# Kernel tuning notes

Hardware: AMD Instinct MI355X
Metric: run time of the kernel (lower is better)

The kernel has to match this reference:

```python
import jax, jax.numpy as jnp
import numpy as np

N_NODES = 100000
N_EDGES = 1600000
N_FEAT = 128
HIDDEN = 64
N_LAYERS = 3


def setup_inputs() -> dict:
    key = jax.random.key(0)
    ks = jax.random.split(key, 8)
    x = jax.random.normal(ks[0], (N_NODES, N_FEAT), dtype=jnp.float32)
    edge_index = jax.random.randint(ks[1], (2, N_EDGES), 0, N_NODES, dtype=jnp.int64)
    s_emb = 1.0 / np.sqrt(N_FEAT)
    s_h = 1.0 / np.sqrt(HIDDEN)
    W_emb = jax.random.uniform(ks[2], (N_FEAT, HIDDEN), jnp.float32, -s_emb, s_emb)
    b_emb = jax.random.uniform(ks[3], (HIDDEN,), jnp.float32, -s_emb, s_emb)
    Ws = jax.random.uniform(ks[4], (N_LAYERS, HIDDEN, HIDDEN), jnp.float32, -s_h, s_h)
    bs = jax.random.uniform(ks[5], (N_LAYERS, HIDDEN), jnp.float32, -s_h, s_h)
    return {"x": x, "edge_index": edge_index, "W_emb": W_emb, "b_emb": b_emb,
            "Ws": Ws, "bs": bs}


def gcn_conv(h, src, dst, W, b, deg_inv_sqrt):
    # GCNConv with self-loops and symmetric normalization (PyG semantics):
    # out_i = sum_{j->i} d_i^{-1/2} d_j^{-1/2} (h_j W) + d_i^{-1} (h_i W) + b
    hw = h @ W                                   # [N, H]
    norm = deg_inv_sqrt[src] * deg_inv_sqrt[dst]  # [E]
    msg = hw[src] * norm[:, None]                 # [E, H] gather
    agg = jax.ops.segment_sum(msg, dst, num_segments=N_NODES)  # scatter-add
    agg = agg + hw * (deg_inv_sqrt * deg_inv_sqrt)[:, None]    # self-loop term
    return agg + b


def reference(x, edge_index, W_emb, b_emb, Ws, bs):
    src, dst = edge_index[0], edge_index[1]
    # degree with self-loops (edge weight 1), shared by every layer
    deg = jnp.zeros((N_NODES,), x.dtype).at[dst].add(1.0) + 1.0
    deg_inv_sqrt = jax.lax.rsqrt(deg)

    h = x @ W_emb + b_emb  # embedding Linear
    for i in range(N_LAYERS):
        h = jax.nn.relu(gcn_conv(h, src, dst, Ws[i], bs[i], deg_inv_sqrt))
    return h
```

## Files before the change

### kernel.cpp

```cpp
#include <hip/hip_runtime.h>
#include <hip/hip_fp16.h>
#include <math.h>

#define NN 100000
#define NE 1600000
#define NF 128
#define NH 64
#define NBUCK 196
#define CHA 8192
#define CAP 10240

__global__ __launch_bounds__(256) void zero_bcnt(int* bcnt) {
    int t = threadIdx.x;
    if (t < NBUCK) bcnt[t] = 0;
}

__global__ __launch_bounds__(256) void part_bucket2(const int* __restrict__ src,
                                                    const int* __restrict__ dst,
                                                    int* __restrict__ bcnt,
                                                    int* __restrict__ tmp, int E) {
    __shared__ int hist[NBUCK];
    __shared__ int base[NBUCK];
    int t = threadIdx.x;
    int e0 = blockIdx.x * CHA;
    int e1 = min(e0 + CHA, E);
    if (t < NBUCK) hist[t] = 0;
    __syncthreads();
    for (int i = e0 + t; i < e1; i += 256) {
        atomicAdd(&hist[dst[i] >> 9], 1);
    }
    __syncthreads();
    if (t < NBUCK) {
        int h = hist[t];
        base[t] = h ? atomicAdd(&bcnt[t], h) : 0;
        hist[t] = 0;
    }
    __syncthreads();
    for (int i = e0 + t; i < e1; i += 256) {
        int d = dst[i];
        int b = d >> 9;
        int r = atomicAdd(&hist[b], 1);
        tmp[b * CAP + base[b] + r] = ((d & 511) << 17) | src[i];
    }
}

__global__ __launch_bounds__(256) void scan_buckets(const int* __restrict__ bcnt,
                                                    int* __restrict__ cbase,
                                                    int* __restrict__ rowptr) {
    __shared__ int s[256];
    int t = threadIdx.x;
    s[t] = (t < NBUCK) ? bcnt[t] : 0;
    __syncthreads();
    for (int off = 1; off < 256; off <<= 1) {
        int v = (t >= off) ? s[t - off] : 0;
        __syncthreads();
        s[t] += v;
        __syncthreads();
    }
    if (t < NBUCK) cbase[t] = (t == 0) ? 0 : s[t - 1];
    if (t == 0) rowptr[NN] = NE;
}

__global__ __launch_bounds__(256) void bucket_finalize(const int* __restrict__ bcnt,
                                                       const int* __restrict__ cbase,
                                                       const int* __restrict__ tmp,
                                                       int* __restrict__ rowptr,
                                                       float* __restrict__ dsq,
                                                       int* __restrict__ csr_src) {
    __shared__ int ebuf[CAP];
    __shared__ int hcnt[512];
    __shared__ int hoff[512];
    __shared__ int s[256];
    int b = blockIdx.x, t = threadIdx.x;
    int cb = bcnt[b];
    int base = cbase[b];
    const int* tsrc = tmp + b * CAP;
    for (int i = t; i < cb; i += 256) ebuf[i] = tsrc[i];
    hcnt[t] = 0;
    hcnt[t + 256] = 0;
    __syncthreads();
    for (int i = t; i < cb; i += 256) atomicAdd(&hcnt[ebuf[i] >> 17], 1);
    __syncthreads();
    int c0 = hcnt[2 * t], c1 = hcnt[2 * t + 1];
    s[t] = c0 + c1;
    __syncthreads();
    for (int off = 1; off < 256; off <<= 1) {
        int v = (t >= off) ? s[t - off] : 0;
        __syncthreads();
        s[t] += v;
        __syncthreads();
    }
    int pb = (t == 0) ? 0 : s[t - 1];
    hoff[2 * t] = pb;
    hoff[2 * t + 1] = pb + c0;
    __syncthreads();
    int nodelo = b << 9;
    int nnodes = min(512, NN - nodelo);
    for (int i = t; i < nnodes; i += 256) {
        rowptr[nodelo + i] = base + hoff[i];
        dsq[nodelo + i] = rsqrtf((float)hcnt[i] + 1.0f);
    }
    __syncthreads();
    for (int i = t; i < cb; i += 256) {
        int e = ebuf[i];
        int dlow = e >> 17;
        int p = atomicAdd(&hoff[dlow], 1);
        csr_src[base + p] = e & 0x1FFFF;
    }
}

__global__ __launch_bounds__(256) void combine_w(const float* __restrict__ We,
                                                 const float* __restrict__ be,
                                                 const float* __restrict__ W0,
                                                 float* __restrict__ Wc,
                                                 float* __restrict__ bc) {
    __shared__ float w0[NH * NH];
    int t = threadIdx.x;
    for (int i = t; i < NH * NH; i += 256) w0[i] = W0[i];
    __syncthreads();
    int row = blockIdx.x * 4 + (t >> 6);
    int col = t & 63;
    float a = 0.f;
#pragma unroll 8
    for (int k = 0; k < NH; ++k) a += We[row * NH + k] * w0[k * NH + col];
    Wc[row * NH + col] = a;
    if (blockIdx.x == 0 && t < NH) {
        float s = 0.f;
        for (int k = 0; k < NH; ++k) s += be[k] * w0[k * NH + t];
        bc[t] = s;
    }
}

__global__ __launch_bounds__(256) void fuse0_gemm(const float* __restrict__ x,
                                                  const float* __restrict__ Wc,
                                                  const float* __restrict__ bc,
                                                  const float* __restrict__ dsq,
                                                  __half* __restrict__ hws) {
    __shared__ float tile[16 * NF];
    __shared__ float red[4][16][NH];
    int t = threadIdx.x;
    int lane = t & 63;
    int wave = __builtin_amdgcn_readfirstlane(t >> 6);
    int row0 = blockIdx.x * 16;

    const float4* xsrc = (const float4*)(x + (size_t)row0 * NF);
    float4* t4 = (float4*)tile;
    t4[t] = xsrc[t];
    t4[t + 256] = xsrc[t + 256];

    float Wreg[32];
#pragma unroll
    for (int kk = 0; kk < 32; ++kk) Wreg[kk] = Wc[(wave * 32 + kk) * NH + lane];
    __syncthreads();

    float acc[16];
#pragma unroll
    for (int r = 0; r < 16; ++r) {
        const float4* rp = (const float4*)(tile + r * NF + wave * 32);
        float a = 0.f;
#pragma unroll
        for (int q = 0; q < 8; ++q) {
            float4 v = rp[q];
            a += v.x * Wreg[q * 4 + 0];
            a += v.y * Wreg[q * 4 + 1];
            a += v.z * Wreg[q * 4 + 2];
            a += v.w * Wreg[q * 4 + 3];
        }
        acc[r] = a;
    }
#pragma unroll
    for (int r = 0; r < 16; ++r) red[wave][r][lane] = acc[r];
    __syncthreads();
#pragma unroll
    for (int i = 0; i < 4; ++i) {
        int o = i * 256 + t;
        int r = o >> 6, c = o & 63;
        float s = red[0][r][c] + red[1][r][c] + red[2][r][c] + red[3][r][c];
        int row = row0 + r;
        hws[(size_t)row * NH + c] = __float2half((s + bc[c]) * dsq[row]);
    }
}

__global__ __launch_bounds__(256) void layer_gemm(const float* __restrict__ h,
                                                  const float* __restrict__ W,
                                                  const float* __restrict__ dsq,
                                                  __half* __restrict__ hws) {
    __shared__ float tile[16 * NH];
    __shared__ float red[4][16][NH];
    int t = threadIdx.x;
    int lane = t & 63;
    int wave = __builtin_amdgcn_readfirstlane(t >> 6);
    int row0 = blockIdx.x * 16;

    const float4* hsrc = (const float4*)(h + (size_t)row0 * NH);
    float4* t4 = (float4*)tile;
    t4[t] = hsrc[t];

    float Wreg[16];
#pragma unroll
    for (int kk = 0; kk < 16; ++kk) Wreg[kk] = W[(wave * 16 + kk) * NH + lane];
    __syncthreads();

    float acc[16];
#pragma unroll
    for (int r = 0; r < 16; ++r) {
        const float4* rp = (const float4*)(tile + r * NH + wave * 16);
        float a = 0.f;
#pragma unroll
        for (int q = 0; q < 4; ++q) {
            float4 v = rp[q];
            a += v.x * Wreg[q * 4 + 0];
            a += v.y * Wreg[q * 4 + 1];
            a += v.z * Wreg[q * 4 + 2];
            a += v.w * Wreg[q * 4 + 3];
        }
        acc[r] = a;
    }
#pragma unroll
    for (int r = 0; r < 16; ++r) red[wave][r][lane] = acc[r];
    __syncthreads();
#pragma unroll
    for (int i = 0; i < 4; ++i) {
        int o = i * 256 + t;
        int r = o >> 6, c = o & 63;
        float s = red[0][r][c] + red[1][r][c] + red[2][r][c] + red[3][r][c];
        int row = row0 + r;
        hws[(size_t)row * NH + c] = __float2half(s * dsq[row]);
    }
}

__global__ __launch_bounds__(256) void gather_agg(const int* __restrict__ rowptr,
                                                  const int* __restrict__ csr_src,
                                                  const __half* __restrict__ hws,
                                                  const float* __restrict__ dsq,
                                                  const float* __restrict__ b,
                                                  float* __restrict__ outbuf, int n) {
    int node = blockIdx.x * 4 + (threadIdx.x >> 6);
    int lane = threadIdx.x & 63;
    if (node >= n) return;
    int g  = lane >> 3;
    int fl = (lane & 7) << 3;
    int beg = rowptr[node], end = rowptr[node + 1];

    float a0 = 0.f, a1 = 0.f, a2 = 0.f, a3 = 0.f;
    float a4 = 0.f, a5 = 0.f, a6 = 0.f, a7 = 0.f;

#define ADDROW(sidx)                                                         \
    {                                                                        \
        uint4 rv = *(const uint4*)(hws + (size_t)(sidx) * NH + fl);          \
        float2 f0 = __half22float2(*(const __half2*)&rv.x);                  \
        float2 f1 = __half22float2(*(const __half2*)&rv.y);                  \
        float2 f2 = __half22float2(*(const __half2*)&rv.z);                  \
        float2 f3 = __half22float2(*(const __half2*)&rv.w);                  \
        a0 += f0.x; a1 += f0.y; a2 += f1.x; a3 += f1.y;                      \
        a4 += f2.x; a5 += f2.y; a6 += f3.x; a7 += f3.y;                      \
    }

    if (g == 0) ADDROW(node);
    int jend = beg + ((end - beg) & ~7);
#pragma unroll 2
    for (int j = beg; j < jend; j += 8) {
        int s = csr_src[j + g];
        ADDROW(s);
    }
    if (jend + g < end) {
        int s = csr_src[jend + g];
        ADDROW(s);
    }
#undef ADDROW

    a0 += __shfl_xor(a0, 8);  a1 += __shfl_xor(a1, 8);
    a2 += __shfl_xor(a2, 8);  a3 += __shfl_xor(a3, 8);
    a4 += __shfl_xor(a4, 8);  a5 += __shfl_xor(a5, 8);
    a6 += __shfl_xor(a6, 8);  a7 += __shfl_xor(a7, 8);
    a0 += __shfl_xor(a0, 16); a1 += __shfl_xor(a1, 16);
    a2 += __shfl_xor(a2, 16); a3 += __shfl_xor(a3, 16);
    a4 += __shfl_xor(a4, 16); a5 += __shfl_xor(a5, 16);
    a6 += __shfl_xor(a6, 16); a7 += __shfl_xor(a7, 16);
    a0 += __shfl_xor(a0, 32); a1 += __shfl_xor(a1, 32);
    a2 += __shfl_xor(a2, 32); a3 += __shfl_xor(a3, 32);
    a4 += __shfl_xor(a4, 32); a5 += __shfl_xor(a5, 32);
    a6 += __shfl_xor(a6, 32); a7 += __shfl_xor(a7, 32);

    if (lane < 8) {
        float ds = dsq[node];
        float4 b0 = *(const float4*)(b + fl);
        float4 b1 = *(const float4*)(b + fl + 4);
        float4 o0, o1;
        o0.x = fmaxf(ds * a0 + b0.x, 0.f);
        o0.y = fmaxf(ds * a1 + b0.y, 0.f);
        o0.z = fmaxf(ds * a2 + b0.z, 0.f);
        o0.w = fmaxf(ds * a3 + b0.w, 0.f);
        o1.x = fmaxf(ds * a4 + b1.x, 0.f);
        o1.y = fmaxf(ds * a5 + b1.y, 0.f);
        o1.z = fmaxf(ds * a6 + b1.z, 0.f);
        o1.w = fmaxf(ds * a7 + b1.w, 0.f);
        *(float4*)(outbuf + (size_t)node * NH + fl) = o0;
        *(float4*)(outbuf + (size_t)node * NH + fl + 4) = o1;
    }
}

extern "C" void kernel_launch(void* const* d_in, const int* in_sizes, int n_in,
                              void* d_out, int out_size, void* d_ws, size_t ws_size,
                              hipStream_t stream) {
    const float* x     = (const float*)d_in[0];
    const int*   ei    = (const int*)d_in[1];
    const float* W_emb = (const float*)d_in[2];
    const float* b_emb = (const float*)d_in[3];
    const float* Ws    = (const float*)d_in[4];
    const float* bs    = (const float*)d_in[5];
    float* out = (float*)d_out;

    const int* src = ei;
    const int* dst = ei + NE;

    char* w = (char*)d_ws;
    int*    bcnt     = (int*)w;               w += 256 * 4;
    int*    cbase    = (int*)w;               w += 256 * 4;
    int*    rowptr   = (int*)w;               w += (NN + 1) * 4;
    float*  dsq      = (float*)w;             w += NN * 4;
    float*  Wc       = (float*)w;             w += NF * NH * 4;
    float*  bc       = (float*)w;             w += NH * 4;
    int*    csr_src  = (int*)w;               w += NE * 4;
    int*    tmp      = (int*)w;               w += (size_t)NBUCK * CAP * 4;
    float*  A        = (float*)w;             w += (size_t)NN * NH * 4;
    __half* Bh       = (__half*)w;

    zero_bcnt<<<1, 256, 0, stream>>>(bcnt);
    part_bucket2<<<(NE + CHA - 1) / CHA, 256, 0, stream>>>(src, dst, bcnt, tmp, NE);
    scan_buckets<<<1, 256, 0, stream>>>(bcnt, cbase, rowptr);
    bucket_finalize<<<NBUCK, 256, 0, stream>>>(bcnt, cbase, tmp, rowptr, dsq, csr_src);

    combine_w<<<NF / 4, 256, 0, stream>>>(W_emb, b_emb, Ws, Wc, bc);

    fuse0_gemm<<<NN / 16, 256, 0, stream>>>(x, Wc, bc, dsq, Bh);
    gather_agg<<<(NN + 3) / 4, 256, 0, stream>>>(rowptr, csr_src, Bh,
                                                 dsq, bs, A, NN);

    for (int l = 1; l < 3; ++l) {
        layer_gemm<<<NN / 16, 256, 0, stream>>>(A, Ws + l * NH * NH, dsq, Bh);
        float* dbuf = (l == 2) ? out : A;
        gather_agg<<<(NN + 3) / 4, 256, 0, stream>>>(rowptr, csr_src, Bh,
                                                     dsq, bs + l * NH, dbuf, NN);
    }
}
```

Before: 295.8 us.

## Fuse next-layer GEMM into gather epilogue and double fuse0 tile rows

The separate layer_gemm kernels are removed. Each gather block now loads the next layer's 64x64 weight into LDS, writes the relu'd aggregated rows to LDS, and computes the next layer's pre-scaled fp16 features directly. This removes the fp32 intermediate write and re-read and two kernel launches per layer. The cost is a 16KB weight load into LDS for every 4-node block and a block-wide sync, which may hurt occupancy. fuse0_gemm also processes 32 rows per block instead of 16.

```diff
diff --git a/kernel.cpp b/kernel.cpp
--- a/kernel.cpp
+++ b/kernel.cpp
@@ -136,26 +136,26 @@
                                                   const float* __restrict__ bc,
                                                   const float* __restrict__ dsq,
                                                   __half* __restrict__ hws) {
-    __shared__ float tile[16 * NF];
-    __shared__ float red[4][16][NH];
+    __shared__ float tile[32 * NF];
+    __shared__ float red[4][32][NH];
     int t = threadIdx.x;
     int lane = t & 63;
     int wave = __builtin_amdgcn_readfirstlane(t >> 6);
-    int row0 = blockIdx.x * 16;
+    int row0 = blockIdx.x * 32;
 
     const float4* xsrc = (const float4*)(x + (size_t)row0 * NF);
     float4* t4 = (float4*)tile;
-    t4[t] = xsrc[t];
-    t4[t + 256] = xsrc[t + 256];
+#pragma unroll
+    for (int i = 0; i < 4; ++i) t4[t + i * 256] = xsrc[t + i * 256];
 
     float Wreg[32];
 #pragma unroll
     for (int kk = 0; kk < 32; ++kk) Wreg[kk] = Wc[(wave * 32 + kk) * NH + lane];
     __syncthreads();
 
-    float acc[16];
-#pragma unroll
-    for (int r = 0; r < 16; ++r) {
+    float acc[32];
+#pragma unroll
+    for (int r = 0; r < 32; ++r) {
         const float4* rp = (const float4*)(tile + r * NF + wave * 32);
         float a = 0.f;
 #pragma unroll
@@ -169,10 +169,10 @@
         acc[r] = a;
     }
 #pragma unroll
-    for (int r = 0; r < 16; ++r) red[wave][r][lane] = acc[r];
-    __syncthreads();
-#pragma unroll
-    for (int i = 0; i < 4; ++i) {
+    for (int r = 0; r < 32; ++r) red[wave][r][lane] = acc[r];
+    __syncthreads();
+#pragma unroll
+    for (int i = 0; i < 8; ++i) {
         int o = i * 256 + t;
         int r = o >> 6, c = o & 63;
         float s = red[0][r][c] + red[1][r][c] + red[2][r][c] + red[3][r][c];
@@ -181,73 +181,41 @@
     }
 }
 
-__global__ __launch_bounds__(256) void layer_gemm(const float* __restrict__ h,
-                                                  const float* __restrict__ W,
-                                                  const float* __restrict__ dsq,
-                                                  __half* __restrict__ hws) {
-    __shared__ float tile[16 * NH];
-    __shared__ float red[4][16][NH];
-    int t = threadIdx.x;
-    int lane = t & 63;
-    int wave = __builtin_amdgcn_readfirstlane(t >> 6);
-    int row0 = blockIdx.x * 16;
-
-    const float4* hsrc = (const float4*)(h + (size_t)row0 * NH);
-    float4* t4 = (float4*)tile;
-    t4[t] = hsrc[t];
-
-    float Wreg[16];
-#pragma unroll
-    for (int kk = 0; kk < 16; ++kk) Wreg[kk] = W[(wave * 16 + kk) * NH + lane];
-    __syncthreads();
-
-    float acc[16];
-#pragma unroll
-    for (int r = 0; r < 16; ++r) {
-        const float4* rp = (const float4*)(tile + r * NH + wave * 16);
-        float a = 0.f;
-#pragma unroll
-        for (int q = 0; q < 4; ++q) {
-            float4 v = rp[q];
-            a += v.x * Wreg[q * 4 + 0];
-            a += v.y * Wreg[q * 4 + 1];
-            a += v.z * Wreg[q * 4 + 2];
-            a += v.w * Wreg[q * 4 + 3];
-        }
-        acc[r] = a;
-    }
-#pragma unroll
-    for (int r = 0; r < 16; ++r) red[wave][r][lane] = acc[r];
-    __syncthreads();
-#pragma unroll
-    for (int i = 0; i < 4; ++i) {
-        int o = i * 256 + t;
-        int r = o >> 6, c = o & 63;
-        float s = red[0][r][c] + red[1][r][c] + red[2][r][c] + red[3][r][c];
-        int row = row0 + r;
-        hws[(size_t)row * NH + c] = __float2half(s * dsq[row]);
-    }
-}
-
-__global__ __launch_bounds__(256) void gather_agg(const int* __restrict__ rowptr,
-                                                  const int* __restrict__ csr_src,
-                                                  const __half* __restrict__ hws,
-                                                  const float* __restrict__ dsq,
-                                                  const float* __restrict__ b,
-                                                  float* __restrict__ outbuf, int n) {
-    int node = blockIdx.x * 4 + (threadIdx.x >> 6);
-    int lane = threadIdx.x & 63;
-    if (node >= n) return;
-    int g  = lane >> 3;
-    int fl = (lane & 7) << 3;
-    int beg = rowptr[node], end = rowptr[node + 1];
-
-    float a0 = 0.f, a1 = 0.f, a2 = 0.f, a3 = 0.f;
-    float a4 = 0.f, a5 = 0.f, a6 = 0.f, a7 = 0.f;
+#define GATHER_BODY                                                          \
+    int t = threadIdx.x;                                                     \
+    int node = blockIdx.x * 4 + (t >> 6);                                    \
+    int lane = t & 63;                                                       \
+    int g = lane >> 3;                                                       \
+    int fl = (lane & 7) << 3;                                                \
+    int beg = rowptr[node], end = rowptr[node + 1];                          \
+    float a0 = 0.f, a1 = 0.f, a2 = 0.f, a3 = 0.f;                            \
+    float a4 = 0.f, a5 = 0.f, a6 = 0.f, a7 = 0.f;                            \
+    if (g == 0) ADDROW(node);                                                \
+    int jend = beg + ((end - beg) & ~7);                                     \
+    _Pragma("unroll 2") for (int j = beg; j < jend; j += 8) {                \
+        int s_ = csr_src[j + g];                                             \
+        ADDROW(s_);                                                          \
+    }                                                                        \
+    if (jend + g < end) {                                                    \
+        int s_ = csr_src[jend + g];                                          \
+        ADDROW(s_);                                                          \
+    }                                                                        \
+    a0 += __shfl_xor(a0, 8);  a1 += __shfl_xor(a1, 8);                       \
+    a2 += __shfl_xor(a2, 8);  a3 += __shfl_xor(a3, 8);                       \
+    a4 += __shfl_xor(a4, 8);  a5 += __shfl_xor(a5, 8);                       \
+    a6 += __shfl_xor(a6, 8);  a7 += __shfl_xor(a7, 8);                       \
+    a0 += __shfl_xor(a0, 16); a1 += __shfl_xor(a1, 16);                      \
+    a2 += __shfl_xor(a2, 16); a3 += __shfl_xor(a3, 16);                      \
+    a4 += __shfl_xor(a4, 16); a5 += __shfl_xor(a5, 16);                      \
+    a6 += __shfl_xor(a6, 16); a7 += __shfl_xor(a7, 16);                      \
+    a0 += __shfl_xor(a0, 32); a1 += __shfl_xor(a1, 32);                      \
+    a2 += __shfl_xor(a2, 32); a3 += __shfl_xor(a3, 32);                      \
+    a4 += __shfl_xor(a4, 32); a5 += __shfl_xor(a5, 32);                      \
+    a6 += __shfl_xor(a6, 32); a7 += __shfl_xor(a7, 32);
 
 #define ADDROW(sidx)                                                         \
     {                                                                        \
-        uint4 rv = *(const uint4*)(hws + (size_t)(sidx) * NH + fl);          \
+        uint4 rv = *(const uint4*)(hws_in + (size_t)(sidx) * NH + fl);       \
         float2 f0 = __half22float2(*(const __half2*)&rv.x);                  \
         float2 f1 = __half22float2(*(const __half2*)&rv.y);                  \
         float2 f2 = __half22float2(*(const __half2*)&rv.z);                  \
@@ -256,32 +224,58 @@
         a4 += f2.x; a5 += f2.y; a6 += f3.x; a7 += f3.y;                      \
     }
 
-    if (g == 0) ADDROW(node);
-    int jend = beg + ((end - beg) & ~7);
-#pragma unroll 2
-    for (int j = beg; j < jend; j += 8) {
-        int s = csr_src[j + g];
-        ADDROW(s);
-    }
-    if (jend + g < end) {
-        int s = csr_src[jend + g];
-        ADDROW(s);
-    }
-#undef ADDROW
-
-    a0 += __shfl_xor(a0, 8);  a1 += __shfl_xor(a1, 8);
-    a2 += __shfl_xor(a2, 8);  a3 += __shfl_xor(a3, 8);
-    a4 += __shfl_xor(a4, 8);  a5 += __shfl_xor(a5, 8);
-    a6 += __shfl_xor(a6, 8);  a7 += __shfl_xor(a7, 8);
-    a0 += __shfl_xor(a0, 16); a1 += __shfl_xor(a1, 16);
-    a2 += __shfl_xor(a2, 16); a3 += __shfl_xor(a3, 16);
-    a4 += __shfl_xor(a4, 16); a5 += __shfl_xor(a5, 16);
-    a6 += __shfl_xor(a6, 16); a7 += __shfl_xor(a7, 16);
-    a0 += __shfl_xor(a0, 32); a1 += __shfl_xor(a1, 32);
-    a2 += __shfl_xor(a2, 32); a3 += __shfl_xor(a3, 32);
-    a4 += __shfl_xor(a4, 32); a5 += __shfl_xor(a5, 32);
-    a6 += __shfl_xor(a6, 32); a7 += __shfl_xor(a7, 32);
-
+__global__ __launch_bounds__(256) void gather_gemm(const int* __restrict__ rowptr,
+                                                   const int* __restrict__ csr_src,
+                                                   const __half* __restrict__ hws_in,
+                                                   const float* __restrict__ dsq,
+                                                   const float* __restrict__ b,
+                                                   const float* __restrict__ Wn,
+                                                   __half* __restrict__ hws_out) {
+    __shared__ float w_lds[NH * NH];
+    __shared__ float h_lds[4][NH];
+    {
+        const float4* ws = (const float4*)Wn;
+        float4* wd = (float4*)w_lds;
+        int tt = threadIdx.x;
+#pragma unroll
+        for (int i = 0; i < 4; ++i) wd[tt + i * 256] = ws[tt + i * 256];
+    }
+    GATHER_BODY
+    float ds = dsq[node];
+    if (lane < 8) {
+        float4 b0 = *(const float4*)(b + fl);
+        float4 b1 = *(const float4*)(b + fl + 4);
+        float4 h0, h1;
+        h0.x = fmaxf(ds * a0 + b0.x, 0.f);
+        h0.y = fmaxf(ds * a1 + b0.y, 0.f);
+        h0.z = fmaxf(ds * a2 + b0.z, 0.f);
+        h0.w = fmaxf(ds * a3 + b0.w, 0.f);
+        h1.x = fmaxf(ds * a4 + b1.x, 0.f);
+        h1.y = fmaxf(ds * a5 + b1.y, 0.f);
+        h1.z = fmaxf(ds * a6 + b1.z, 0.f);
+        h1.w = fmaxf(ds * a7 + b1.w, 0.f);
+        *(float4*)&h_lds[t >> 6][fl] = h0;
+        *(float4*)&h_lds[t >> 6][fl + 4] = h1;
+    }
+    __syncthreads();
+    int r = t >> 6, c = lane;
+    float acc = 0.f;
+#pragma unroll
+    for (int k = 0; k < NH; k += 4) {
+        float4 hv = *(const float4*)&h_lds[r][k];
+        acc += hv.x * w_lds[k * NH + c] + hv.y * w_lds[(k + 1) * NH + c] +
+               hv.z * w_lds[(k + 2) * NH + c] + hv.w * w_lds[(k + 3) * NH + c];
+    }
+    hws_out[(size_t)node * NH + c] = __float2half(acc * ds);
+}
+
+__global__ __launch_bounds__(256) void gather_final(const int* __restrict__ rowptr,
+                                                    const int* __restrict__ csr_src,
+                                                    const __half* __restrict__ hws_in,
+                                                    const float* __restrict__ dsq,
+                                                    const float* __restrict__ b,
+                                                    float* __restrict__ outbuf) {
+    GATHER_BODY
     if (lane < 8) {
         float ds = dsq[node];
         float4 b0 = *(const float4*)(b + fl);
@@ -323,8 +317,8 @@
     float*  bc       = (float*)w;             w += NH * 4;
     int*    csr_src  = (int*)w;               w += NE * 4;
     int*    tmp      = (int*)w;               w += (size_t)NBUCK * CAP * 4;
-    float*  A        = (float*)w;             w += (size_t)NN * NH * 4;
-    __half* Bh       = (__half*)w;
+    __half* Bh0      = (__half*)w;            w += (size_t)NN * NH * 2;
+    __half* Bh1      = (__half*)w;
 
     zero_bcnt<<<1, 256, 0, stream>>>(bcnt);
     part_bucket2<<<(NE + CHA - 1) / CHA, 256, 0, stream>>>(src, dst, bcnt, tmp, NE);
@@ -333,14 +327,12 @@
 
     combine_w<<<NF / 4, 256, 0, stream>>>(W_emb, b_emb, Ws, Wc, bc);
 
-    fuse0_gemm<<<NN / 16, 256, 0, stream>>>(x, Wc, bc, dsq, Bh);
-    gather_agg<<<(NN + 3) / 4, 256, 0, stream>>>(rowptr, csr_src, Bh,
-                                                 dsq, bs, A, NN);
-
-    for (int l = 1; l < 3; ++l) {
-        layer_gemm<<<NN / 16, 256, 0, stream>>>(A, Ws + l * NH * NH, dsq, Bh);
-        float* dbuf = (l == 2) ? out : A;
-        gather_agg<<<(NN + 3) / 4, 256, 0, stream>>>(rowptr, csr_src, Bh,
-                                                     dsq, bs + l * NH, dbuf, NN);
-    }
-}
+    fuse0_gemm<<<NN / 32, 256, 0, stream>>>(x, Wc, bc, dsq, Bh0);
+
+    gather_gemm<<<NN / 4, 256, 0, stream>>>(rowptr, csr_src, Bh0, dsq, bs,
+                                            Ws + 1 * NH * NH, Bh1);
+    gather_gemm<<<NN / 4, 256, 0, stream>>>(rowptr, csr_src, Bh1, dsq, bs + NH,
+                                            Ws + 2 * NH * NH, Bh0);
+    gather_final<<<NN / 4, 256, 0, stream>>>(rowptr, csr_src, Bh0, dsq,
+                                             bs + 2 * NH, out);
+}
```

Result: slower. 311.0 us (+5.1%).

## Store intermediate activations in fp16 and batch neighbor index loads via shuffles

Applied to the files above, without the earlier changes.

Intermediate layer activations between gather and GEMM are now stored as fp16 instead of fp32, halving that write and read traffic. The gather kernel loads up to 64 neighbor indices per wave in one coalesced load and distributes them with shuffles, masking the tail instead of running a separate remainder path. The zero kernel is replaced by hipMemsetAsync. This adds an extra rounding to fp16 of the post-ReLU activations, which costs some accuracy.

```diff
diff --git a/kernel.cpp b/kernel.cpp
--- a/kernel.cpp
+++ b/kernel.cpp
@@ -9,11 +9,6 @@
 #define NBUCK 196
 #define CHA 8192
 #define CAP 10240
-
-__global__ __launch_bounds__(256) void zero_bcnt(int* bcnt) {
-    int t = threadIdx.x;
-    if (t < NBUCK) bcnt[t] = 0;
-}
 
 __global__ __launch_bounds__(256) void part_bucket2(const int* __restrict__ src,
                                                     const int* __restrict__ dst,
@@ -181,7 +176,7 @@
     }
 }
 
-__global__ __launch_bounds__(256) void layer_gemm(const float* __restrict__ h,
+__global__ __launch_bounds__(256) void layer_gemm(const __half* __restrict__ h,
                                                   const float* __restrict__ W,
                                                   const float* __restrict__ dsq,
                                                   __half* __restrict__ hws) {
@@ -192,9 +187,13 @@
     int wave = __builtin_amdgcn_readfirstlane(t >> 6);
     int row0 = blockIdx.x * 16;
 
-    const float4* hsrc = (const float4*)(h + (size_t)row0 * NH);
-    float4* t4 = (float4*)tile;
-    t4[t] = hsrc[t];
+    {
+        uint2 v = ((const uint2*)(h + (size_t)row0 * NH))[t];
+        float2 p0 = __half22float2(*(const __half2*)&v.x);
+        float2 p1 = __half22float2(*(const __half2*)&v.y);
+        float4 f = make_float4(p0.x, p0.y, p1.x, p1.y);
+        *(float4*)&tile[t * 4] = f;
+    }
 
     float Wreg[16];
 #pragma unroll
@@ -229,59 +228,91 @@
     }
 }
 
-__global__ __launch_bounds__(256) void gather_agg(const int* __restrict__ rowptr,
-                                                  const int* __restrict__ csr_src,
-                                                  const __half* __restrict__ hws,
-                                                  const float* __restrict__ dsq,
-                                                  const float* __restrict__ b,
-                                                  float* __restrict__ outbuf, int n) {
-    int node = blockIdx.x * 4 + (threadIdx.x >> 6);
-    int lane = threadIdx.x & 63;
-    if (node >= n) return;
-    int g  = lane >> 3;
-    int fl = (lane & 7) << 3;
-    int beg = rowptr[node], end = rowptr[node + 1];
-
-    float a0 = 0.f, a1 = 0.f, a2 = 0.f, a3 = 0.f;
-    float a4 = 0.f, a5 = 0.f, a6 = 0.f, a7 = 0.f;
-
-#define ADDROW(sidx)                                                         \
+#define ADDROWM(sidx, m)                                                     \
     {                                                                        \
-        uint4 rv = *(const uint4*)(hws + (size_t)(sidx) * NH + fl);          \
+        uint4 rv = *(const uint4*)(hws_in + (size_t)(sidx) * NH + fl);       \
         float2 f0 = __half22float2(*(const __half2*)&rv.x);                  \
         float2 f1 = __half22float2(*(const __half2*)&rv.y);                  \
         float2 f2 = __half22float2(*(const __half2*)&rv.z);                  \
         float2 f3 = __half22float2(*(const __half2*)&rv.w);                  \
-        a0 += f0.x; a1 += f0.y; a2 += f1.x; a3 += f1.y;                      \
-        a4 += f2.x; a5 += f2.y; a6 += f3.x; a7 += f3.y;                      \
-    }
-
-    if (g == 0) ADDROW(node);
-    int jend = beg + ((end - beg) & ~7);
-#pragma unroll 2
-    for (int j = beg; j < jend; j += 8) {
-        int s = csr_src[j + g];
-        ADDROW(s);
-    }
-    if (jend + g < end) {
-        int s = csr_src[jend + g];
-        ADDROW(s);
-    }
-#undef ADDROW
-
-    a0 += __shfl_xor(a0, 8);  a1 += __shfl_xor(a1, 8);
-    a2 += __shfl_xor(a2, 8);  a3 += __shfl_xor(a3, 8);
-    a4 += __shfl_xor(a4, 8);  a5 += __shfl_xor(a5, 8);
-    a6 += __shfl_xor(a6, 8);  a7 += __shfl_xor(a7, 8);
-    a0 += __shfl_xor(a0, 16); a1 += __shfl_xor(a1, 16);
-    a2 += __shfl_xor(a2, 16); a3 += __shfl_xor(a3, 16);
-    a4 += __shfl_xor(a4, 16); a5 += __shfl_xor(a5, 16);
-    a6 += __shfl_xor(a6, 16); a7 += __shfl_xor(a7, 16);
-    a0 += __shfl_xor(a0, 32); a1 += __shfl_xor(a1, 32);
-    a2 += __shfl_xor(a2, 32); a3 += __shfl_xor(a3, 32);
-    a4 += __shfl_xor(a4, 32); a5 += __shfl_xor(a5, 32);
+        a0 += f0.x * (m); a1 += f0.y * (m); a2 += f1.x * (m); a3 += f1.y * (m); \
+        a4 += f2.x * (m); a5 += f2.y * (m); a6 += f3.x * (m); a7 += f3.y * (m); \
+    }
+
+#define GATHER_BODY                                                          \
+    int t = threadIdx.x;                                                     \
+    int node = blockIdx.x * 4 + (t >> 6);                                    \
+    int lane = t & 63;                                                       \
+    int g = lane >> 3;                                                       \
+    int fl = (lane & 7) << 3;                                                \
+    int beg = rowptr[node], end = rowptr[node + 1];                          \
+    int deg = end - beg;                                                     \
+    float a0 = 0.f, a1 = 0.f, a2 = 0.f, a3 = 0.f;                            \
+    float a4 = 0.f, a5 = 0.f, a6 = 0.f, a7 = 0.f;                            \
+    if (g == 0) ADDROWM(node, 1.f);                                          \
+    int idxl = csr_src[min(beg + lane, NE - 1)];                             \
+    _Pragma("unroll")                                                        \
+    for (int k = 0; k < 8; ++k) {                                            \
+        if (k * 8 < deg) {                                                   \
+            int e = k * 8 + g;                                               \
+            int s_ = __shfl(idxl, min(e, deg - 1));                          \
+            float m = (e < deg) ? 1.f : 0.f;                                 \
+            ADDROWM(s_, m);                                                  \
+        }                                                                    \
+    }                                                                        \
+    for (int jb = beg + 64; jb < end; jb += 64) {       \
+        int rem = end - jb;                                                  \
+        int idx2 = csr_src[min(jb + lane, NE - 1)];                          \
+        _Pragma("unroll")                                                    \
+        for (int k = 0; k < 8; ++k) {                                        \
+            if (k * 8 < rem) {                                               \
+                int e = k * 8 + g;                                           \
+                int s_ = __shfl(idx2, min(e, rem - 1));                      \
+                float m = (e < rem) ? 1.f : 0.f;                             \
+                ADDROWM(s_, m);                                              \
+            }                                                                \
+        }                                                                    \
+    }                                                                        \
+    a0 += __shfl_xor(a0, 8);  a1 += __shfl_xor(a1, 8);                       \
+    a2 += __shfl_xor(a2, 8);  a3 += __shfl_xor(a3, 8);                       \
+    a4 += __shfl_xor(a4, 8);  a5 += __shfl_xor(a5, 8);                       \
+    a6 += __shfl_xor(a6, 8);  a7 += __shfl_xor(a7, 8);                       \
+    a0 += __shfl_xor(a0, 16); a1 += __shfl_xor(a1, 16);                      \
+    a2 += __shfl_xor(a2, 16); a3 += __shfl_xor(a3, 16);                      \
+    a4 += __shfl_xor(a4, 16); a5 += __shfl_xor(a5, 16);                      \
+    a6 += __shfl_xor(a6, 16); a7 += __shfl_xor(a7, 16);                      \
+    a0 += __shfl_xor(a0, 32); a1 += __shfl_xor(a1, 32);                      \
+    a2 += __shfl_xor(a2, 32); a3 += __shfl_xor(a3, 32);                      \
+    a4 += __shfl_xor(a4, 32); a5 += __shfl_xor(a5, 32);                      \
     a6 += __shfl_xor(a6, 32); a7 += __shfl_xor(a7, 32);
 
+__global__ __launch_bounds__(256) void gather_h(const int* __restrict__ rowptr,
+                                                const int* __restrict__ csr_src,
+                                                const __half* __restrict__ hws_in,
+                                                const float* __restrict__ dsq,
+                                                const float* __restrict__ b,
+                                                __half* __restrict__ hout) {
+    GATHER_BODY
+    if (lane < 8) {
+        float ds = dsq[node];
+        float4 b0 = *(const float4*)(b + fl);
+        float4 b1 = *(const float4*)(b + fl + 4);
+        __half2 o[4];
+        o[0] = __floats2half2_rn(fmaxf(ds * a0 + b0.x, 0.f), fmaxf(ds * a1 + b0.y, 0.f));
+        o[1] = __floats2half2_rn(fmaxf(ds * a2 + b0.z, 0.f), fmaxf(ds * a3 + b0.w, 0.f));
+        o[2] = __floats2half2_rn(fmaxf(ds * a4 + b1.x, 0.f), fmaxf(ds * a5 + b1.y, 0.f));
+        o[3] = __floats2half2_rn(fmaxf(ds * a6 + b1.z, 0.f), fmaxf(ds * a7 + b1.w, 0.f));
+        *(uint4*)(hout + (size_t)node * NH + fl) = *(const uint4*)o;
+    }
+}
+
+__global__ __launch_bounds__(256) void gather_out(const int* __restrict__ rowptr,
+                                                  const int* __restrict__ csr_src,
+                                                  const __half* __restrict__ hws_in,
+                                                  const float* __restrict__ dsq,
+                                                  const float* __restrict__ b,
+                                                  float* __restrict__ outbuf) {
+    GATHER_BODY
     if (lane < 8) {
         float ds = dsq[node];
         float4 b0 = *(const float4*)(b + fl);
@@ -323,10 +354,10 @@
     float*  bc       = (float*)w;             w += NH * 4;
     int*    csr_src  = (int*)w;               w += NE * 4;
     int*    tmp      = (int*)w;               w += (size_t)NBUCK * CAP * 4;
-    float*  A        = (float*)w;             w += (size_t)NN * NH * 4;
-    __half* Bh       = (__half*)w;
-
-    zero_bcnt<<<1, 256, 0, stream>>>(bcnt);
+    __half* Bh       = (__half*)w;            w += (size_t)NN * NH * 2;
+    __half* H16      = (__half*)w;
+
+    hipMemsetAsync(bcnt, 0, 256 * 4, stream);
     part_bucket2<<<(NE + CHA - 1) / CHA, 256, 0, stream>>>(src, dst, bcnt, tmp, NE);
     scan_buckets<<<1, 256, 0, stream>>>(bcnt, cbase, rowptr);
     bucket_finalize<<<NBUCK, 256, 0, stream>>>(bcnt, cbase, tmp, rowptr, dsq, csr_src);
@@ -334,13 +365,11 @@
     combine_w<<<NF / 4, 256, 0, stream>>>(W_emb, b_emb, Ws, Wc, bc);
 
     fuse0_gemm<<<NN / 16, 256, 0, stream>>>(x, Wc, bc, dsq, Bh);
-    gather_agg<<<(NN + 3) / 4, 256, 0, stream>>>(rowptr, csr_src, Bh,
-                                                 dsq, bs, A, NN);
-
-    for (int l = 1; l < 3; ++l) {
-        layer_gemm<<<NN / 16, 256, 0, stream>>>(A, Ws + l * NH * NH, dsq, Bh);
-        float* dbuf = (l == 2) ? out : A;
-        gather_agg<<<(NN + 3) / 4, 256, 0, stream>>>(rowptr, csr_src, Bh,
-                                                     dsq, bs + l * NH, dbuf, NN);
-    }
-}
+
+    gather_h<<<NN / 4, 256, 0, stream>>>(rowptr, csr_src, Bh, dsq, bs, H16);
+    layer_gemm<<<NN / 16, 256, 0, stream>>>(H16, Ws + 1 * NH * NH, dsq, Bh);
+    gather_h<<<NN / 4, 256, 0, stream>>>(rowptr, csr_src, Bh, dsq, bs + NH, H16);
+    layer_gemm<<<NN / 16, 256, 0, stream>>>(H16, Ws + 2 * NH * NH, dsq, Bh);
+    gather_out<<<NN / 4, 256, 0, stream>>>(rowptr, csr_src, Bh, dsq,
+                                           bs + 2 * NH, out);
+}
```

Result: no change. 296.4 us (+0.2%).
